# Kernel optimization log

Measured on AMD Instinct MI355X. Metric: run time of the kernel, lower is better.

## Reference

```python
import jax, jax.numpy as jnp
import numpy as np

N = 100000
E = 3200000
IN_C, HID_C, OUT_C = 128, 16, 1


def setup_inputs() -> dict:
    key = jax.random.key(0)
    k1, k2, k3, k4, k5, k6 = jax.random.split(key, 6)
    x = jax.random.normal(k1, (N, IN_C), dtype=jnp.float32)
    edge_index = jax.random.randint(k2, (2, E), 0, N, dtype=jnp.int64)
    # Glorot-style init like PyG GCNConv
    W1 = jax.random.normal(k3, (IN_C, HID_C), dtype=jnp.float32) / np.sqrt(IN_C)
    b1 = jnp.zeros((HID_C,), dtype=jnp.float32)
    W2 = jax.random.normal(k4, (HID_C, OUT_C), dtype=jnp.float32) / np.sqrt(HID_C)
    b2 = jnp.zeros((OUT_C,), dtype=jnp.float32)
    return {"x": x, "edge_index": edge_index, "W1": W1, "b1": b1, "W2": W2, "b2": b2}


def _gcn_conv(x, W, b, src, dst, norm):
    # Linear transform first (PyG default flow: transform then aggregate)
    h = x @ W                                  # [N, C_out]
    msg = h[src] * norm[:, None]               # gather + edge-wise scale, [E+N, C_out]
    out = jax.ops.segment_sum(msg, dst, num_segments=N)  # scatter-add, [N, C_out]
    return out + b


def reference(x, edge_index, W1, b1, W2, b2):
    # GCNConv: add self-loops, symmetric normalization D^-1/2 A D^-1/2
    loop = jnp.arange(N, dtype=edge_index.dtype)
    src = jnp.concatenate([edge_index[0], loop])   # [E+N]
    dst = jnp.concatenate([edge_index[1], loop])   # [E+N]
    deg = jax.ops.segment_sum(jnp.ones_like(dst, dtype=x.dtype), dst, num_segments=N)
    dinv = jnp.where(deg > 0, jax.lax.rsqrt(deg), 0.0)
    norm = dinv[src] * dinv[dst]                   # [E+N]

    h = _gcn_conv(x, W1, b1, src, dst, norm)
    h = jax.nn.relu(h)
    # dropout is identity in eval mode (training=False)
    h = _gcn_conv(h, W2, b2, src, dst, norm)
    return jax.nn.sigmoid(h).squeeze()             # [N]
```

## Files before the change

kernel.cpp:

```cpp
#include <hip/hip_runtime.h>
#include <hip/hip_bf16.h>
#include <math.h>

typedef unsigned int u32;

constexpr int N_NODES = 100000;
constexpr int N_EDGES = 3200000;
constexpr int IN_C    = 128;
constexpr int HID_C   = 16;

constexpr int BKT_SHIFT = 11;
constexpr int BKT_NODES = 1 << BKT_SHIFT;
constexpr int NB  = (N_NODES + BKT_NODES - 1) / BKT_NODES;
constexpr int CAP = 67000;
constexpr int EPB = (N_EDGES + 255) / 256;
constexpr int K_SEG = 8;

__global__ void k_zero(u32* __restrict__ cursor) {
    int i = threadIdx.x;
    if (i < NB) cursor[i] = 0u;
}

__global__ __launch_bounds__(1024) void k_bucket(const int* __restrict__ src,
                                                 const int* __restrict__ dst,
                                                 u32* __restrict__ cursor,
                                                 u32* __restrict__ barr) {
    __shared__ u32 cnt[NB];
    __shared__ u32 base[NB];
    const int e0 = blockIdx.x * EPB;
    const int e1 = min(N_EDGES, e0 + EPB);
    for (int i = threadIdx.x; i < NB; i += blockDim.x) cnt[i] = 0u;
    __syncthreads();
    for (int e = e0 + threadIdx.x; e < e1; e += blockDim.x)
        atomicAdd(&cnt[((u32)dst[e]) >> BKT_SHIFT], 1u);
    __syncthreads();
    for (int i = threadIdx.x; i < NB; i += blockDim.x)
        base[i] = atomicAdd(&cursor[i], cnt[i]);
    __syncthreads();
    for (int e = e0 + threadIdx.x; e < e1; e += blockDim.x) {
        u32 d = (u32)dst[e];
        u32 b = d >> BKT_SHIFT;
        u32 pos = atomicAdd(&base[b], 1u);
        if (pos < (u32)CAP)
            barr[(size_t)b * CAP + pos] = ((d & (BKT_NODES - 1)) << 17) | (u32)src[e];
    }
}

__global__ __launch_bounds__(1024) void k_hist(const u32* __restrict__ barr,
                                               const u32* __restrict__ cursor,
                                               u32* __restrict__ seghist) {
    __shared__ u32 h[BKT_NODES];
    const int b = blockIdx.x / K_SEG, s = blockIdx.x % K_SEG;
    const u32 sz = min(cursor[b], (u32)CAP);
    for (int i = threadIdx.x; i < BKT_NODES; i += blockDim.x) h[i] = 0u;
    __syncthreads();
    const u32 e0 = sz * (u32)s / K_SEG, e1 = sz * (u32)(s + 1) / K_SEG;
    const u32* p = barr + (size_t)b * CAP;
    for (u32 e = e0 + threadIdx.x; e < e1; e += blockDim.x)
        atomicAdd(&h[p[e] >> 17], 1u);
    __syncthreads();
    u32* o = seghist + (size_t)(b * K_SEG + s) * BKT_NODES;
    for (int i = threadIdx.x; i < BKT_NODES; i += blockDim.x) o[i] = h[i];
}

__global__ void k_bucketscan(const u32* __restrict__ cursor, u32* __restrict__ bucketBase,
                             int* __restrict__ rowptr) {
    if (threadIdx.x == 0) {
        u32 t = 0;
        for (int b = 0; b < NB; ++b) { bucketBase[b] = t; t += min(cursor[b], (u32)CAP); }
        rowptr[N_NODES] = (int)t;
    }
}

__global__ __launch_bounds__(1024) void k_scan(u32* __restrict__ seghist,
                                               const u32* __restrict__ bucketBase,
                                               int* __restrict__ rowptr,
                                               float* __restrict__ dinv) {
    __shared__ u32 sa[BKT_NODES], sb[BKT_NODES];
    const int b = blockIdx.x;
    const int nbase = b << BKT_SHIFT;
    for (int n = threadIdx.x; n < BKT_NODES; n += blockDim.x) {
        u32 t = 0;
#pragma unroll
        for (int s = 0; s < K_SEG; ++s) {
            size_t idx = (size_t)(b * K_SEG + s) * BKT_NODES + n;
            u32 v = seghist[idx];
            seghist[idx] = t;
            t += v;
        }
        sa[n] = t;
        if (nbase + n < N_NODES) dinv[nbase + n] = rsqrtf(1.0f + (float)t);
    }
    __syncthreads();
    u32 *pa = sa, *pb = sb;
    for (int off = 1; off < BKT_NODES; off <<= 1) {
        for (int n = threadIdx.x; n < BKT_NODES; n += blockDim.x)
            pb[n] = pa[n] + (n >= off ? pa[n - off] : 0u);
        __syncthreads();
        u32* t = pa; pa = pb; pb = t;
    }
    const u32 bb = bucketBase[b];
    for (int n = threadIdx.x; n < BKT_NODES; n += blockDim.x) {
        u32 excl = bb + (n ? pa[n - 1] : 0u);
        if (nbase + n < N_NODES) rowptr[nbase + n] = (int)excl;
#pragma unroll
        for (int s = 0; s < K_SEG; ++s)
            seghist[(size_t)(b * K_SEG + s) * BKT_NODES + n] += excl;
    }
}

__global__ __launch_bounds__(1024) void k_scatter(const u32* __restrict__ barr,
                                                  const u32* __restrict__ cursor,
                                                  const u32* __restrict__ seghist,
                                                  int* __restrict__ adj) {
    __shared__ u32 cur[BKT_NODES];
    const int b = blockIdx.x / K_SEG, s = blockIdx.x % K_SEG;
    const u32 sz = min(cursor[b], (u32)CAP);
    const u32* sbase = seghist + (size_t)(b * K_SEG + s) * BKT_NODES;
    for (int i = threadIdx.x; i < BKT_NODES; i += blockDim.x) cur[i] = sbase[i];
    __syncthreads();
    const u32 e0 = sz * (u32)s / K_SEG, e1 = sz * (u32)(s + 1) / K_SEG;
    const u32* p = barr + (size_t)b * CAP;
    for (u32 e = e0 + threadIdx.x; e < e1; e += blockDim.x) {
        u32 ent = p[e];
        u32 pos = atomicAdd(&cur[ent >> 17], 1u);
        adj[pos] = (int)(ent & 0x1FFFFu);
    }
}

__global__ void k_gemm1(const float* __restrict__ x, const float* __restrict__ W1,
                        const float* __restrict__ dinv, __hip_bfloat16* __restrict__ g1b,
                        float* __restrict__ g1f) {
    __shared__ float sW[IN_C * HID_C];
    for (int t = threadIdx.x; t < IN_C * HID_C; t += blockDim.x) sW[t] = W1[t];
    __syncthreads();

    int t = blockIdx.x * blockDim.x + threadIdx.x;
    int node = t >> 4;
    int c = t & 15;
    if (node >= N_NODES) return;

    const float4* xr = (const float4*)(x + (size_t)node * IN_C);
    float acc = 0.f;
#pragma unroll
    for (int j = 0; j < IN_C / 4; ++j) {
        float4 v = xr[j];
        acc = fmaf(v.x, sW[(4 * j + 0) * HID_C + c], acc);
        acc = fmaf(v.y, sW[(4 * j + 1) * HID_C + c], acc);
        acc = fmaf(v.z, sW[(4 * j + 2) * HID_C + c], acc);
        acc = fmaf(v.w, sW[(4 * j + 3) * HID_C + c], acc);
    }
    float val = acc * dinv[node];
    int o = node * HID_C + c;
    g1b[o] = __float2bfloat16(val);
    g1f[o] = val;
}

__global__ void k_agg1(const int* __restrict__ rowptr, const int* __restrict__ adj,
                       const u32* __restrict__ g1u, const float* __restrict__ g1f,
                       const float* __restrict__ dinv, const float* __restrict__ b1,
                       const float* __restrict__ W2, float* __restrict__ g2) {
    int t = blockIdx.x * blockDim.x + threadIdx.x;
    int g = t >> 3, l = t & 7;
    if (g >= N_NODES) return;
    int base = rowptr[g], end = rowptr[g + 1];
    float2 self = ((const float2*)g1f)[g * 8 + l];
    float a0 = self.x, a1 = self.y;
    int k = base;
    for (; k + 4 <= end; k += 4) {
        int s0 = adj[k], s1 = adj[k + 1], s2 = adj[k + 2], s3 = adj[k + 3];
        u32 v0 = g1u[s0 * 8 + l], v1 = g1u[s1 * 8 + l];
        u32 v2 = g1u[s2 * 8 + l], v3 = g1u[s3 * 8 + l];
        a0 += __uint_as_float(v0 << 16);
        a1 += __uint_as_float(v0 & 0xFFFF0000u);
        a0 += __uint_as_float(v1 << 16);
        a1 += __uint_as_float(v1 & 0xFFFF0000u);
        a0 += __uint_as_float(v2 << 16);
        a1 += __uint_as_float(v2 & 0xFFFF0000u);
        a0 += __uint_as_float(v3 << 16);
        a1 += __uint_as_float(v3 & 0xFFFF0000u);
    }
    for (; k < end; ++k) {
        u32 v = g1u[adj[k] * 8 + l];
        a0 += __uint_as_float(v << 16);
        a1 += __uint_as_float(v & 0xFFFF0000u);
    }
    float di = dinv[g];
    float2 bb = ((const float2*)b1)[l];
    float2 w  = ((const float2*)W2)[l];
    float h0 = fmaxf(fmaf(a0, di, bb.x), 0.f);
    float h1 = fmaxf(fmaf(a1, di, bb.y), 0.f);
    float part = h0 * w.x + h1 * w.y;
    part += __shfl_xor(part, 1);
    part += __shfl_xor(part, 2);
    part += __shfl_xor(part, 4);
    if (l == 0) g2[g] = part * di;
}

__global__ void k_agg2(const int* __restrict__ rowptr, const int* __restrict__ adj,
                       const float* __restrict__ g2, const float* __restrict__ dinv,
                       const float* __restrict__ b2, float* __restrict__ out) {
    int t = blockIdx.x * blockDim.x + threadIdx.x;
    int g = t >> 2, l = t & 3;
    if (g >= N_NODES) return;
    int base = rowptr[g], end = rowptr[g + 1];
    float acc = (l == 0) ? g2[g] : 0.f;
    for (int k = base + l; k < end; k += 4) acc += g2[adj[k]];
    acc += __shfl_xor(acc, 1);
    acc += __shfl_xor(acc, 2);
    if (l == 0) {
        float v = fmaf(acc, dinv[g], b2[0]);
        out[g] = 1.0f / (1.0f + __expf(-v));
    }
}

extern "C" void kernel_launch(void* const* d_in, const int* in_sizes, int n_in,
                              void* d_out, int out_size, void* d_ws, size_t ws_size,
                              hipStream_t stream) {
    const float* x    = (const float*)d_in[0];
    const int*   edge = (const int*)d_in[1];
    const float* W1   = (const float*)d_in[2];
    const float* b1   = (const float*)d_in[3];
    const float* W2   = (const float*)d_in[4];
    const float* b2   = (const float*)d_in[5];
    float*       out  = (float*)d_out;

    const int* src = edge;
    const int* dst = edge + N_EDGES;

    char* w = (char*)d_ws;
    auto alloc = [&](size_t bytes) { char* r = w; w += (bytes + 255) & ~(size_t)255; return r; };
    u32*   barr       = (u32*)  alloc((size_t)NB * CAP * 4);
    u32*   seghist    = (u32*)  alloc((size_t)NB * K_SEG * BKT_NODES * 4);
    u32*   cursor     = (u32*)  alloc(NB * 4);
    u32*   bucketBase = (u32*)  alloc(NB * 4);
    int*   rowptr     = (int*)  alloc((size_t)(N_NODES + 1) * 4);
    float* dinv       = (float*)alloc((size_t)N_NODES * 4);
    int*   adj        = (int*)  alloc((size_t)N_EDGES * 4);
    float*          g1f = (float*)barr;
    float*          g2  = (float*)(barr + (size_t)N_NODES * HID_C);
    __hip_bfloat16* g1b = (__hip_bfloat16*)seghist;
    const u32*      g1u = (const u32*)seghist;

    const int gGemm = (N_NODES * HID_C + 255) / 256;
    const int gAgg1 = (N_NODES * 8 + 255) / 256;
    const int gAgg2 = (N_NODES * 4 + 255) / 256;

    hipLaunchKernelGGL(k_zero,       dim3(1),            dim3(64),   0, stream, cursor);
    hipLaunchKernelGGL(k_bucket,     dim3(256),          dim3(1024), 0, stream, src, dst, cursor, barr);
    hipLaunchKernelGGL(k_hist,       dim3(NB * K_SEG),   dim3(1024), 0, stream, barr, cursor, seghist);
    hipLaunchKernelGGL(k_bucketscan, dim3(1),            dim3(64),   0, stream, cursor, bucketBase, rowptr);
    hipLaunchKernelGGL(k_scan,       dim3(NB),           dim3(1024), 0, stream, seghist, bucketBase, rowptr, dinv);
    hipLaunchKernelGGL(k_scatter,    dim3(NB * K_SEG),   dim3(1024), 0, stream, barr, cursor, seghist, adj);
    hipLaunchKernelGGL(k_gemm1,      dim3(gGemm),        dim3(256),  0, stream, x, W1, dinv, g1b, g1f);
    hipLaunchKernelGGL(k_agg1,       dim3(gAgg1),        dim3(256),  0, stream, rowptr, adj, g1u, g1f, dinv, b1, W2, g2);
    hipLaunchKernelGGL(k_agg2,       dim3(gAgg2),        dim3(256),  0, stream, rowptr, adj, g2, dinv, b2, out);
}
```

Before: 246.3 us.

## Cache edges in registers, fold bucket scan, tile gemm1 via LDS, drop fp32 copy

k_bucket now loads each thread's dst/src edges into registers once, so the second pass no longer reads them from global memory again. The single-thread bucketscan kernel is removed and each k_scan block sums the bucket sizes before it, which saves one launch. k_gemm1 is restructured to stage 16 rows of x and a transposed W1 in padded shared memory and read both as float4, and it no longer writes the fp32 copy of the layer-1 features. k_agg1 now reads its self term from the bf16 array, which slightly changes precision for that term.

```diff
diff --git a/kernel.cpp b/kernel.cpp
--- a/kernel.cpp
+++ b/kernel.cpp
@@ -14,6 +14,7 @@
 constexpr int NB  = (N_NODES + BKT_NODES - 1) / BKT_NODES;
 constexpr int CAP = 67000;
 constexpr int EPB = (N_EDGES + 255) / 256;
+constexpr int MAXE = (EPB + 1023) / 1024;
 constexpr int K_SEG = 8;
 
 __global__ void k_zero(u32* __restrict__ cursor) {
@@ -29,20 +30,29 @@
     __shared__ u32 base[NB];
     const int e0 = blockIdx.x * EPB;
     const int e1 = min(N_EDGES, e0 + EPB);
+    u32 myD[MAXE], myS[MAXE];
+#pragma unroll
+    for (int i = 0; i < MAXE; ++i) {
+        int e = e0 + threadIdx.x + i * 1024;
+        if (e < e1) { myD[i] = (u32)dst[e]; myS[i] = (u32)src[e]; }
+        else myD[i] = 0xFFFFFFFFu;
+    }
     for (int i = threadIdx.x; i < NB; i += blockDim.x) cnt[i] = 0u;
     __syncthreads();
-    for (int e = e0 + threadIdx.x; e < e1; e += blockDim.x)
-        atomicAdd(&cnt[((u32)dst[e]) >> BKT_SHIFT], 1u);
+#pragma unroll
+    for (int i = 0; i < MAXE; ++i)
+        if (myD[i] != 0xFFFFFFFFu) atomicAdd(&cnt[myD[i] >> BKT_SHIFT], 1u);
     __syncthreads();
     for (int i = threadIdx.x; i < NB; i += blockDim.x)
         base[i] = atomicAdd(&cursor[i], cnt[i]);
     __syncthreads();
-    for (int e = e0 + threadIdx.x; e < e1; e += blockDim.x) {
-        u32 d = (u32)dst[e];
-        u32 b = d >> BKT_SHIFT;
+#pragma unroll
+    for (int i = 0; i < MAXE; ++i) {
+        if (myD[i] == 0xFFFFFFFFu) continue;
+        u32 b = myD[i] >> BKT_SHIFT;
         u32 pos = atomicAdd(&base[b], 1u);
         if (pos < (u32)CAP)
-            barr[(size_t)b * CAP + pos] = ((d & (BKT_NODES - 1)) << 17) | (u32)src[e];
+            barr[(size_t)b * CAP + pos] = ((myD[i] & (BKT_NODES - 1)) << 17) | myS[i];
     }
 }
 
@@ -63,22 +73,20 @@
     for (int i = threadIdx.x; i < BKT_NODES; i += blockDim.x) o[i] = h[i];
 }
 
-__global__ void k_bucketscan(const u32* __restrict__ cursor, u32* __restrict__ bucketBase,
-                             int* __restrict__ rowptr) {
-    if (threadIdx.x == 0) {
-        u32 t = 0;
-        for (int b = 0; b < NB; ++b) { bucketBase[b] = t; t += min(cursor[b], (u32)CAP); }
-        rowptr[N_NODES] = (int)t;
-    }
-}
-
 __global__ __launch_bounds__(1024) void k_scan(u32* __restrict__ seghist,
-                                               const u32* __restrict__ bucketBase,
+                                               const u32* __restrict__ cursor,
                                                int* __restrict__ rowptr,
                                                float* __restrict__ dinv) {
     __shared__ u32 sa[BKT_NODES], sb[BKT_NODES];
+    __shared__ u32 s_bb;
     const int b = blockIdx.x;
     const int nbase = b << BKT_SHIFT;
+    if (threadIdx.x == 0) {
+        u32 t = 0;
+        for (int q = 0; q < b; ++q) t += min(cursor[q], (u32)CAP);
+        s_bb = t;
+        if (b == NB - 1) rowptr[N_NODES] = (int)(t + min(cursor[b], (u32)CAP));
+    }
     for (int n = threadIdx.x; n < BKT_NODES; n += blockDim.x) {
         u32 t = 0;
 #pragma unroll
@@ -99,7 +107,7 @@
         __syncthreads();
         u32* t = pa; pa = pb; pb = t;
     }
-    const u32 bb = bucketBase[b];
+    const u32 bb = s_bb;
     for (int n = threadIdx.x; n < BKT_NODES; n += blockDim.x) {
         u32 excl = bb + (n ? pa[n - 1] : 0u);
         if (nbase + n < N_NODES) rowptr[nbase + n] = (int)excl;
@@ -128,44 +136,60 @@
     }
 }
 
-__global__ void k_gemm1(const float* __restrict__ x, const float* __restrict__ W1,
-                        const float* __restrict__ dinv, __hip_bfloat16* __restrict__ g1b,
-                        float* __restrict__ g1f) {
-    __shared__ float sW[IN_C * HID_C];
-    for (int t = threadIdx.x; t < IN_C * HID_C; t += blockDim.x) sW[t] = W1[t];
-    __syncthreads();
-
-    int t = blockIdx.x * blockDim.x + threadIdx.x;
-    int node = t >> 4;
-    int c = t & 15;
-    if (node >= N_NODES) return;
-
-    const float4* xr = (const float4*)(x + (size_t)node * IN_C);
+constexpr int NPB = 16;
+constexpr int XPAD = 132;
+__global__ __launch_bounds__(256) void k_gemm1(const float* __restrict__ x,
+                                               const float* __restrict__ W1,
+                                               const float* __restrict__ dinv,
+                                               __hip_bfloat16* __restrict__ g1b) {
+    __shared__ float sx[NPB * XPAD];
+    __shared__ float swT[HID_C * XPAD];
+    const int nbase = blockIdx.x * NPB;
+    {
+        const float4* xs = (const float4*)(x + (size_t)nbase * IN_C);
+#pragma unroll
+        for (int k = 0; k < 2; ++k) {
+            int idx = threadIdx.x + k * 256;
+            int row = idx >> 5, col4 = idx & 31;
+            float4 v = xs[idx];
+            ((float4*)(sx + row * XPAD))[col4] = v;
+        }
+    }
+    for (int t = threadIdx.x; t < IN_C * HID_C; t += 256) {
+        int j = t >> 4, c = t & 15;
+        swT[c * XPAD + j] = W1[t];
+    }
+    __syncthreads();
+
+    const int n = threadIdx.x >> 4;
+    const int c = threadIdx.x & 15;
+    const float4* row = (const float4*)(sx + n * XPAD);
+    const float4* wc  = (const float4*)(swT + c * XPAD);
     float acc = 0.f;
 #pragma unroll
     for (int j = 0; j < IN_C / 4; ++j) {
-        float4 v = xr[j];
-        acc = fmaf(v.x, sW[(4 * j + 0) * HID_C + c], acc);
-        acc = fmaf(v.y, sW[(4 * j + 1) * HID_C + c], acc);
-        acc = fmaf(v.z, sW[(4 * j + 2) * HID_C + c], acc);
-        acc = fmaf(v.w, sW[(4 * j + 3) * HID_C + c], acc);
-    }
-    float val = acc * dinv[node];
-    int o = node * HID_C + c;
-    g1b[o] = __float2bfloat16(val);
-    g1f[o] = val;
+        float4 v = row[j];
+        float4 w = wc[j];
+        acc = fmaf(v.x, w.x, acc);
+        acc = fmaf(v.y, w.y, acc);
+        acc = fmaf(v.z, w.z, acc);
+        acc = fmaf(v.w, w.w, acc);
+    }
+    const int node = nbase + n;
+    g1b[node * HID_C + c] = __float2bfloat16(acc * dinv[node]);
 }
 
 __global__ void k_agg1(const int* __restrict__ rowptr, const int* __restrict__ adj,
-                       const u32* __restrict__ g1u, const float* __restrict__ g1f,
+                       const u32* __restrict__ g1u,
                        const float* __restrict__ dinv, const float* __restrict__ b1,
                        const float* __restrict__ W2, float* __restrict__ g2) {
     int t = blockIdx.x * blockDim.x + threadIdx.x;
     int g = t >> 3, l = t & 7;
     if (g >= N_NODES) return;
     int base = rowptr[g], end = rowptr[g + 1];
-    float2 self = ((const float2*)g1f)[g * 8 + l];
-    float a0 = self.x, a1 = self.y;
+    u32 sv = g1u[g * 8 + l];
+    float a0 = __uint_as_float(sv << 16);
+    float a1 = __uint_as_float(sv & 0xFFFF0000u);
     int k = base;
     for (; k + 4 <= end; k += 4) {
         int s0 = adj[k], s1 = adj[k + 1], s2 = adj[k + 2], s3 = adj[k + 3];
@@ -233,26 +257,23 @@
     u32*   barr       = (u32*)  alloc((size_t)NB * CAP * 4);
     u32*   seghist    = (u32*)  alloc((size_t)NB * K_SEG * BKT_NODES * 4);
     u32*   cursor     = (u32*)  alloc(NB * 4);
-    u32*   bucketBase = (u32*)  alloc(NB * 4);
     int*   rowptr     = (int*)  alloc((size_t)(N_NODES + 1) * 4);
     float* dinv       = (float*)alloc((size_t)N_NODES * 4);
     int*   adj        = (int*)  alloc((size_t)N_EDGES * 4);
-    float*          g1f = (float*)barr;
-    float*          g2  = (float*)(barr + (size_t)N_NODES * HID_C);
+    float*          g2  = (float*)barr;
     __hip_bfloat16* g1b = (__hip_bfloat16*)seghist;
     const u32*      g1u = (const u32*)seghist;
 
-    const int gGemm = (N_NODES * HID_C + 255) / 256;
+    const int gGemm = N_NODES / NPB;
     const int gAgg1 = (N_NODES * 8 + 255) / 256;
     const int gAgg2 = (N_NODES * 4 + 255) / 256;
 
-    hipLaunchKernelGGL(k_zero,       dim3(1),            dim3(64),   0, stream, cursor);
-    hipLaunchKernelGGL(k_bucket,     dim3(256),          dim3(1024), 0, stream, src, dst, cursor, barr);
-    hipLaunchKernelGGL(k_hist,       dim3(NB * K_SEG),   dim3(1024), 0, stream, barr, cursor, seghist);
-    hipLaunchKernelGGL(k_bucketscan, dim3(1),            dim3(64),   0, stream, cursor, bucketBase, rowptr);
-    hipLaunchKernelGGL(k_scan,       dim3(NB),           dim3(1024), 0, stream, seghist, bucketBase, rowptr, dinv);
-    hipLaunchKernelGGL(k_scatter,    dim3(NB * K_SEG),   dim3(1024), 0, stream, barr, cursor, seghist, adj);
-    hipLaunchKernelGGL(k_gemm1,      dim3(gGemm),        dim3(256),  0, stream, x, W1, dinv, g1b, g1f);
-    hipLaunchKernelGGL(k_agg1,       dim3(gAgg1),        dim3(256),  0, stream, rowptr, adj, g1u, g1f, dinv, b1, W2, g2);
-    hipLaunchKernelGGL(k_agg2,       dim3(gAgg2),        dim3(256),  0, stream, rowptr, adj, g2, dinv, b2, out);
-}
+    hipLaunchKernelGGL(k_zero,    dim3(1),          dim3(64),   0, stream, cursor);
+    hipLaunchKernelGGL(k_bucket,  dim3(256),        dim3(1024), 0, stream, src, dst, cursor, barr);
+    hipLaunchKernelGGL(k_hist,    dim3(NB * K_SEG), dim3(1024), 0, stream, barr, cursor, seghist);
+    hipLaunchKernelGGL(k_scan,    dim3(NB),         dim3(1024), 0, stream, seghist, cursor, rowptr, dinv);
+    hipLaunchKernelGGL(k_scatter, dim3(NB * K_SEG), dim3(1024), 0, stream, barr, cursor, seghist, adj);
+    hipLaunchKernelGGL(k_gemm1,   dim3(gGemm),      dim3(256),  0, stream, x, W1, dinv, g1b);
+    hipLaunchKernelGGL(k_agg1,    dim3(gAgg1),      dim3(256),  0, stream, rowptr, adj, g1u, dinv, b1, W2, g2);
+    hipLaunchKernelGGL(k_agg2,    dim3(gAgg2),      dim3(256),  0, stream, rowptr, adj, g2, dinv, b2, out);
+}
```

Measured after the change: 224.9 us. 1.1x faster.
